# Performance work log

Measured on AMD Instinct MI355X. Metric: run time of the kernel, lower is better.

## Reference

```python
import jax, jax.numpy as jnp
import numpy as np


def setup_inputs() -> dict:
    key = jax.random.key(0)
    ks = jax.random.split(key, 7)
    B, S, IN, OUT = 4, 2048, 4096, 4096
    R_DEC, R_TR = 1024, 64
    return {
        "x": jax.random.normal(ks[0], (B, S, IN), dtype=jnp.float32),
        "siva_u_t": jax.random.normal(ks[1], (OUT, R_TR), dtype=jnp.float32) * 0.02,
        "siva_u_d": jax.random.normal(ks[2], (OUT, R_DEC - R_TR), dtype=jnp.float32) * 0.02,
        "siva_s": jax.random.uniform(ks[3], (R_DEC,), dtype=jnp.float32),
        "siva_v_t": jax.random.normal(ks[4], (R_TR, IN), dtype=jnp.float32) * 0.02,
        "siva_v_d": jax.random.normal(ks[5], (R_DEC - R_TR, IN), dtype=jnp.float32) * 0.02,
        "bias": jax.random.normal(ks[6], (OUT,), dtype=jnp.float32) * 0.02,
    }


def reference(x, siva_u_t, siva_u_d, siva_s, siva_v_t, siva_v_d, bias):
    # Faithful to torch: weight = (cat(U_t, U_d, dim=1) * S) @ cat(V_t, V_d, dim=0)
    siva_u = jnp.concatenate((siva_u_t, siva_u_d), axis=1)   # [out, r]
    siva_v = jnp.concatenate((siva_v_t, siva_v_d), axis=0)   # [r, in]
    weight = (siva_u * siva_s) @ siva_v                       # [out, in]
    # F.linear: x @ weight.T + bias
    return jnp.einsum("bsi,oi->bso", x, weight) + bias
```

## Files before the change

### kernel.cpp

```cpp
#include <hip/hip_runtime.h>
#include <cstdint>


#define BM 128
#define BN 128
#define BK 32

typedef __bf16 bf16x8 __attribute__((ext_vector_type(8)));
typedef float f32x4 __attribute__((ext_vector_type(4)));

__device__ __forceinline__ unsigned short f32_to_bf16(float f) {
    union { float f; uint32_t u; } v; v.f = f;
    uint32_t u = v.u;
    u += 0x7FFF + ((u >> 16) & 1);
    return (unsigned short)(u >> 16);
}

__global__ void cast_f32_bf16(const float* __restrict__ src,
                              unsigned short* __restrict__ dst, int n4) {
    int i = blockIdx.x * blockDim.x + threadIdx.x;
    if (i >= n4) return;
    float4 v = ((const float4*)src)[i];
    ushort4 o;
    o.x = f32_to_bf16(v.x); o.y = f32_to_bf16(v.y);
    o.z = f32_to_bf16(v.z); o.w = f32_to_bf16(v.w);
    ((ushort4*)dst)[i] = o;
}

__global__ void build_u(const float* __restrict__ u_t, const float* __restrict__ u_d,
                        const float* __restrict__ s, unsigned short* __restrict__ ub,
                        int n4) {
    int i = blockIdx.x * blockDim.x + threadIdx.x;
    if (i >= n4) return;
    int e = i * 4;
    int o = e >> 10;
    int r = e & 1023;
    float4 u;
    if (r < 64) u = *(const float4*)(u_t + (size_t)o * 64 + r);
    else        u = *(const float4*)(u_d + (size_t)o * 960 + (r - 64));
    float4 sv = *(const float4*)(s + r);
    ushort4 w;
    w.x = f32_to_bf16(u.x * sv.x);
    w.y = f32_to_bf16(u.y * sv.y);
    w.z = f32_to_bf16(u.z * sv.z);
    w.w = f32_to_bf16(u.w * sv.w);
    ((ushort4*)ub)[i] = w;
}

__device__ __forceinline__ void stage16(const unsigned short* g, unsigned short* l) {
    __builtin_amdgcn_global_load_lds(
        (const __attribute__((address_space(1))) uint32_t*)g,
        (__attribute__((address_space(3))) uint32_t*)l, 16, 0, 0);
}

__global__ __launch_bounds__(256, 4)
void gemm_a(const unsigned short* __restrict__ A, const unsigned short* __restrict__ B,
            float* __restrict__ Yp) {
    __shared__ unsigned short ldsA[BM * BK];
    __shared__ unsigned short ldsB[BN * BK];

    const int tid  = threadIdx.x;
    const int wave = tid >> 6, lane = tid & 63;
    const int wm = wave >> 1, wn = wave & 1;
    const int q = lane >> 4, l16 = lane & 15;

    const int b = blockIdx.x + (blockIdx.y << 3);
    const int c = b & 7;
    const int t = b >> 3;
    const int tx = t & 7;
    const int ty = ((t >> 3) << 3) + c;
    const int m0 = ty * BM, n0 = tx * BN;
    const int kbase = blockIdx.z * 2048;

    f32x4 acc[4][4] = {};

    const int rowc = tid >> 2;
    const int colc = (tid & 3) << 3;
    const unsigned short* pA0 = A + (size_t)(m0 + rowc) * 4096 + kbase + colc;
    const unsigned short* pA1 = pA0 + (size_t)64 * 4096;
    const unsigned short* pB0 = B + (size_t)(n0 + rowc) * 4096 + kbase + colc;
    const unsigned short* pB1 = pB0 + (size_t)64 * 4096;
    unsigned short* lA0 = ldsA + tid * 8;
    unsigned short* lA1 = ldsA + (tid + 256) * 8;
    unsigned short* lB0 = ldsB + tid * 8;
    unsigned short* lB1 = ldsB + (tid + 256) * 8;

    const int raBase = (wm * 64 + l16) * BK + q * 8;
    const int rbBase = (wn * 64 + l16) * BK + q * 8;

    for (int kt = 0; kt < 64; ++kt) {
        stage16(pA0, lA0);
        stage16(pA1, lA1);
        stage16(pB0, lB0);
        stage16(pB1, lB1);
        pA0 += BK; pA1 += BK; pB0 += BK; pB1 += BK;
        asm volatile("s_waitcnt vmcnt(0)" ::: "memory");
        __syncthreads();

        bf16x8 af[4], bfr[4];
#pragma unroll
        for (int i = 0; i < 4; ++i) {
            af[i]  = *(const bf16x8*)(ldsA + raBase + i * (16 * BK));
            bfr[i] = *(const bf16x8*)(ldsB + rbBase + i * (16 * BK));
        }
#pragma unroll
        for (int mt = 0; mt < 4; ++mt)
#pragma unroll
            for (int nt = 0; nt < 4; ++nt)
                acc[mt][nt] = __builtin_amdgcn_mfma_f32_16x16x32_bf16(
                    af[mt], bfr[nt], acc[mt][nt], 0, 0, 0);
        __syncthreads();
    }

    float* out = Yp + (size_t)blockIdx.z * 8192 * 1024;
#pragma unroll
    for (int mt = 0; mt < 4; ++mt)
#pragma unroll
        for (int nt = 0; nt < 4; ++nt) {
            const int col = n0 + wn * 64 + nt * 16 + l16;
            const int rbase = m0 + wm * 64 + mt * 16 + q * 4;
#pragma unroll
            for (int i = 0; i < 4; ++i)
                out[(size_t)(rbase + i) * 1024 + col] = acc[mt][nt][i];
        }
}

__global__ void reduce_y(const float* __restrict__ p0, const float* __restrict__ p1,
                         unsigned short* __restrict__ y, int n4) {
    int i = blockIdx.x * blockDim.x + threadIdx.x;
    if (i >= n4) return;
    float4 a = ((const float4*)p0)[i];
    float4 b = ((const float4*)p1)[i];
    ushort4 w;
    w.x = f32_to_bf16(a.x + b.x);
    w.y = f32_to_bf16(a.y + b.y);
    w.z = f32_to_bf16(a.z + b.z);
    w.w = f32_to_bf16(a.w + b.w);
    ((ushort4*)y)[i] = w;
}

__global__ __launch_bounds__(256, 4)
void gemm_b(const unsigned short* __restrict__ A, const unsigned short* __restrict__ B,
            float* __restrict__ C, const float* __restrict__ bias) {
    __shared__ unsigned short ldsA[BM * BK];
    __shared__ unsigned short ldsB[BN * BK];

    const int tid  = threadIdx.x;
    const int wave = tid >> 6, lane = tid & 63;
    const int wm = wave >> 1, wn = wave & 1;
    const int q = lane >> 4, l16 = lane & 15;

    const int b = blockIdx.x + (blockIdx.y << 5);
    const int c = b & 7;
    const int t = b >> 3;
    const int tx = t & 31;
    const int ty = ((t >> 5) << 3) + c;
    const int m0 = ty * BM, n0 = tx * BN;

    const int K = 1024, N = 4096;
    f32x4 acc[4][4] = {};

    const int rowc = tid >> 2;
    const int colc = (tid & 3) << 3;
    const unsigned short* pA0 = A + (size_t)(m0 + rowc) * K + colc;
    const unsigned short* pA1 = pA0 + (size_t)64 * K;
    const unsigned short* pB0 = B + (size_t)(n0 + rowc) * K + colc;
    const unsigned short* pB1 = pB0 + (size_t)64 * K;
    unsigned short* lA0 = ldsA + tid * 8;
    unsigned short* lA1 = ldsA + (tid + 256) * 8;
    unsigned short* lB0 = ldsB + tid * 8;
    unsigned short* lB1 = ldsB + (tid + 256) * 8;

    const int raBase = (wm * 64 + l16) * BK + q * 8;
    const int rbBase = (wn * 64 + l16) * BK + q * 8;

    for (int kt = 0; kt < K / BK; ++kt) {
        stage16(pA0, lA0);
        stage16(pA1, lA1);
        stage16(pB0, lB0);
        stage16(pB1, lB1);
        pA0 += BK; pA1 += BK; pB0 += BK; pB1 += BK;
        asm volatile("s_waitcnt vmcnt(0)" ::: "memory");
        __syncthreads();

        bf16x8 af[4], bfr[4];
#pragma unroll
        for (int i = 0; i < 4; ++i) {
            af[i]  = *(const bf16x8*)(ldsA + raBase + i * (16 * BK));
            bfr[i] = *(const bf16x8*)(ldsB + rbBase + i * (16 * BK));
        }
#pragma unroll
        for (int mt = 0; mt < 4; ++mt)
#pragma unroll
            for (int nt = 0; nt < 4; ++nt)
                acc[mt][nt] = __builtin_amdgcn_mfma_f32_16x16x32_bf16(
                    af[mt], bfr[nt], acc[mt][nt], 0, 0, 0);
        __syncthreads();
    }

#pragma unroll
    for (int mt = 0; mt < 4; ++mt)
#pragma unroll
        for (int nt = 0; nt < 4; ++nt) {
            const int col = n0 + wn * 64 + nt * 16 + l16;
            const int rbase = m0 + wm * 64 + mt * 16 + q * 4;
            const float bv = bias[col];
#pragma unroll
            for (int i = 0; i < 4; ++i)
                C[(size_t)(rbase + i) * N + col] = acc[mt][nt][i] + bv;
        }
}

extern "C" void kernel_launch(void* const* d_in, const int* in_sizes, int n_in,
                              void* d_out, int out_size, void* d_ws, size_t ws_size,
                              hipStream_t stream) {
    const float* x    = (const float*)d_in[0];
    const float* u_t  = (const float*)d_in[1];
    const float* u_d  = (const float*)d_in[2];
    const float* s    = (const float*)d_in[3];
    const float* v_t  = (const float*)d_in[4];
    const float* v_d  = (const float*)d_in[5];
    const float* bias = (const float*)d_in[6];
    float* out = (float*)d_out;

    const int M = 8192, IN = 4096, R = 1024, OUT = 4096;

    char* ws = (char*)d_ws;
    float*          Yp = (float*)ws;
    unsigned short* xb = (unsigned short*)(ws + (size_t)(64 << 20));
    unsigned short* Vb = (unsigned short*)(ws + (size_t)(128 << 20));
    unsigned short* Ub = (unsigned short*)(ws + (size_t)(136 << 20));
    unsigned short* Yb = (unsigned short*)(ws + (size_t)(144 << 20));

    {
        int n4 = M * IN / 4;
        cast_f32_bf16<<<(n4 + 255) / 256, 256, 0, stream>>>(x, xb, n4);
    }
    {
        int n4 = 64 * IN / 4;
        cast_f32_bf16<<<(n4 + 255) / 256, 256, 0, stream>>>(v_t, Vb, n4);
    }
    {
        int n4 = 960 * IN / 4;
        cast_f32_bf16<<<(n4 + 255) / 256, 256, 0, stream>>>(v_d, Vb + 64 * IN, n4);
    }
    {
        int n4 = OUT * R / 4;
        build_u<<<(n4 + 255) / 256, 256, 0, stream>>>(u_t, u_d, s, Ub, n4);
    }

    gemm_a<<<dim3(R / BN, M / BM, 2), 256, 0, stream>>>(xb, Vb, Yp);
    {
        int n4 = M * R / 4;
        reduce_y<<<(n4 + 255) / 256, 256, 0, stream>>>(Yp, Yp + (size_t)M * R, Yb, n4);
    }
    gemm_b<<<dim3(OUT / BN, M / BM), 256, 0, stream>>>(Yb, Ub, out, bias);
}
```

Measured before the change: 434.1 us.

## Replace both GEMMs with a double-buffered 256x256 tile kernel with swizzled LDS

Replaces the two 128x128 single-buffered GEMM kernels with one templated 256x256-tile, 512-thread kernel. It uses BK=64 split into two halves, double-buffered LDS with async global-to-LDS prefetch interleaved between MFMA phases, and XOR-swizzled LDS layout to avoid bank conflicts. It also adds s_setprio around MFMA bursts and a new block-index swizzle. This targets the load-wait-compute serialization and low arithmetic intensity of the old kernels, at the cost of higher register and LDS use and fewer resident blocks.

After: 413.9 us. -4.6%, faster.

```diff
diff --git a/kernel.cpp b/kernel.cpp
--- a/kernel.cpp
+++ b/kernel.cpp
@@ -1,10 +1,6 @@
 #include <hip/hip_runtime.h>
 #include <cstdint>
 
-
-#define BM 128
-#define BN 128
-#define BK 32
 
 typedef __bf16 bf16x8 __attribute__((ext_vector_type(8)));
 typedef float f32x4 __attribute__((ext_vector_type(4)));
@@ -47,84 +43,6 @@
     ((ushort4*)ub)[i] = w;
 }
 
-__device__ __forceinline__ void stage16(const unsigned short* g, unsigned short* l) {
-    __builtin_amdgcn_global_load_lds(
-        (const __attribute__((address_space(1))) uint32_t*)g,
-        (__attribute__((address_space(3))) uint32_t*)l, 16, 0, 0);
-}
-
-__global__ __launch_bounds__(256, 4)
-void gemm_a(const unsigned short* __restrict__ A, const unsigned short* __restrict__ B,
-            float* __restrict__ Yp) {
-    __shared__ unsigned short ldsA[BM * BK];
-    __shared__ unsigned short ldsB[BN * BK];
-
-    const int tid  = threadIdx.x;
-    const int wave = tid >> 6, lane = tid & 63;
-    const int wm = wave >> 1, wn = wave & 1;
-    const int q = lane >> 4, l16 = lane & 15;
-
-    const int b = blockIdx.x + (blockIdx.y << 3);
-    const int c = b & 7;
-    const int t = b >> 3;
-    const int tx = t & 7;
-    const int ty = ((t >> 3) << 3) + c;
-    const int m0 = ty * BM, n0 = tx * BN;
-    const int kbase = blockIdx.z * 2048;
-
-    f32x4 acc[4][4] = {};
-
-    const int rowc = tid >> 2;
-    const int colc = (tid & 3) << 3;
-    const unsigned short* pA0 = A + (size_t)(m0 + rowc) * 4096 + kbase + colc;
-    const unsigned short* pA1 = pA0 + (size_t)64 * 4096;
-    const unsigned short* pB0 = B + (size_t)(n0 + rowc) * 4096 + kbase + colc;
-    const unsigned short* pB1 = pB0 + (size_t)64 * 4096;
-    unsigned short* lA0 = ldsA + tid * 8;
-    unsigned short* lA1 = ldsA + (tid + 256) * 8;
-    unsigned short* lB0 = ldsB + tid * 8;
-    unsigned short* lB1 = ldsB + (tid + 256) * 8;
-
-    const int raBase = (wm * 64 + l16) * BK + q * 8;
-    const int rbBase = (wn * 64 + l16) * BK + q * 8;
-
-    for (int kt = 0; kt < 64; ++kt) {
-        stage16(pA0, lA0);
-        stage16(pA1, lA1);
-        stage16(pB0, lB0);
-        stage16(pB1, lB1);
-        pA0 += BK; pA1 += BK; pB0 += BK; pB1 += BK;
-        asm volatile("s_waitcnt vmcnt(0)" ::: "memory");
-        __syncthreads();
-
-        bf16x8 af[4], bfr[4];
-#pragma unroll
-        for (int i = 0; i < 4; ++i) {
-            af[i]  = *(const bf16x8*)(ldsA + raBase + i * (16 * BK));
-            bfr[i] = *(const bf16x8*)(ldsB + rbBase + i * (16 * BK));
-        }
-#pragma unroll
-        for (int mt = 0; mt < 4; ++mt)
-#pragma unroll
-            for (int nt = 0; nt < 4; ++nt)
-                acc[mt][nt] = __builtin_amdgcn_mfma_f32_16x16x32_bf16(
-                    af[mt], bfr[nt], acc[mt][nt], 0, 0, 0);
-        __syncthreads();
-    }
-
-    float* out = Yp + (size_t)blockIdx.z * 8192 * 1024;
-#pragma unroll
-    for (int mt = 0; mt < 4; ++mt)
-#pragma unroll
-        for (int nt = 0; nt < 4; ++nt) {
-            const int col = n0 + wn * 64 + nt * 16 + l16;
-            const int rbase = m0 + wm * 64 + mt * 16 + q * 4;
-#pragma unroll
-            for (int i = 0; i < 4; ++i)
-                out[(size_t)(rbase + i) * 1024 + col] = acc[mt][nt][i];
-        }
-}
-
 __global__ void reduce_y(const float* __restrict__ p0, const float* __restrict__ p1,
                          unsigned short* __restrict__ y, int n4) {
     int i = blockIdx.x * blockDim.x + threadIdx.x;
@@ -139,76 +57,154 @@
     ((ushort4*)y)[i] = w;
 }
 
-__global__ __launch_bounds__(256, 4)
-void gemm_b(const unsigned short* __restrict__ A, const unsigned short* __restrict__ B,
-            float* __restrict__ C, const float* __restrict__ bias) {
-    __shared__ unsigned short ldsA[BM * BK];
-    __shared__ unsigned short ldsB[BN * BK];
-
-    const int tid  = threadIdx.x;
-    const int wave = tid >> 6, lane = tid & 63;
-    const int wm = wave >> 1, wn = wave & 1;
+__device__ __forceinline__ void stage16(const unsigned short* g, unsigned short* l) {
+    __builtin_amdgcn_global_load_lds(
+        (const __attribute__((address_space(1))) uint32_t*)g,
+        (__attribute__((address_space(3))) uint32_t*)l, 16, 0, 0);
+}
+
+
+#define STAGE_A(bb, kh, t_) do {                                              \
+    const unsigned short* s_ = pAsrc + (t_) * 64 + (kh) * 32;                 \
+    unsigned short* d_ = ldsA_dst + (bb) * 32768 + (kh) * 8192;               \
+    stage16(s_, d_);                                                          \
+    stage16(s_ + (size_t)128 * LD, d_ + 4096);                                \
+} while (0)
+
+#define STAGE_B(bb, kh, t_) do {                                              \
+    const unsigned short* s_ = pBsrc + (t_) * 64 + (kh) * 32;                 \
+    unsigned short* d_ = ldsB_dst + (bb) * 32768 + (kh) * 8192;               \
+    stage16(s_, d_);                                                          \
+    stage16(s_ + (size_t)128 * LD, d_ + 4096);                                \
+} while (0)
+
+#define READ_AF(bb, ks, mh) do {                                              \
+    const unsigned short* p_ = lds + (bb) * 32768 + (ks) * 8192 + aoff + (mh) * 2048; \
+    af[0] = *(const bf16x8*)(p_);                                             \
+    af[1] = *(const bf16x8*)(p_ + 512);                                       \
+    af[2] = *(const bf16x8*)(p_ + 1024);                                      \
+    af[3] = *(const bf16x8*)(p_ + 1536);                                      \
+} while (0)
+
+#define READ_BF(bb, ks) do {                                                  \
+    const unsigned short* p_ = lds + (bb) * 32768 + 16384 + (ks) * 8192 + boff; \
+    bfr[0] = *(const bf16x8*)(p_);                                            \
+    bfr[1] = *(const bf16x8*)(p_ + 512);                                      \
+    bfr[2] = *(const bf16x8*)(p_ + 1024);                                     \
+    bfr[3] = *(const bf16x8*)(p_ + 1536);                                     \
+} while (0)
+
+#define MFMA16(mh) do {                                                       \
+    __builtin_amdgcn_s_barrier();                                             \
+    __builtin_amdgcn_sched_barrier(0);                                        \
+    __builtin_amdgcn_s_setprio(1);                                            \
+    _Pragma("unroll") for (int i_ = 0; i_ < 4; ++i_) {                        \
+        _Pragma("unroll") for (int n_ = 0; n_ < 4; ++n_) {                    \
+            acc[(mh) * 4 + i_][n_] = __builtin_amdgcn_mfma_f32_16x16x32_bf16( \
+                af[i_], bfr[n_], acc[(mh) * 4 + i_][n_], 0, 0, 0);            \
+        }                                                                     \
+    }                                                                         \
+    __builtin_amdgcn_s_setprio(0);                                            \
+    __builtin_amdgcn_sched_barrier(0);                                        \
+} while (0)
+
+#define PHASE_END do {                                                        \
+    __builtin_amdgcn_s_barrier();                                             \
+    __builtin_amdgcn_sched_barrier(0);                                        \
+} while (0)
+
+#define BODY(t_, bb) do {                                                     \
+    const int tp1 = (t_) + 1, tp2 = (t_) + 2;                                 \
+    bf16x8 af[4], bfr[4];                                                     \
+                                                          \
+    READ_AF(bb, 0, 0); READ_BF(bb, 0);                                        \
+    if (tp1 < KTILES) STAGE_A((bb) ^ 1, 1, tp1);                              \
+    MFMA16(0); PHASE_END;                                                     \
+                                                          \
+    READ_AF(bb, 0, 1);                                                        \
+    if (tp1 < KTILES) STAGE_B((bb) ^ 1, 1, tp1);                              \
+    MFMA16(1); PHASE_END;                                                     \
+                                                          \
+    READ_AF(bb, 1, 0); READ_BF(bb, 1);                                        \
+    if (tp2 < KTILES) STAGE_A((bb), 0, tp2);                                  \
+    MFMA16(0); PHASE_END;                                                     \
+                                                          \
+    READ_AF(bb, 1, 1);                                                        \
+    if (tp2 < KTILES) STAGE_B((bb), 0, tp2);                                  \
+    MFMA16(1);                                                                \
+    if (tp2 < KTILES)      asm volatile("s_waitcnt vmcnt(4)" ::: "memory");   \
+    else if (tp1 < KTILES) asm volatile("s_waitcnt vmcnt(0)" ::: "memory");   \
+    PHASE_END;                                                                \
+} while (0)
+
+template<int KTILES, int LD, int NTX, bool BIAS, int SPLITK>
+__global__ __launch_bounds__(512, 2)
+void gemm256(const unsigned short* __restrict__ A, const unsigned short* __restrict__ B,
+             float* __restrict__ C, const float* __restrict__ bias) {
+    static_assert((KTILES % 2) == 0 && KTILES >= 4, "KTILES even >= 4");
+    __shared__ unsigned short lds[65536];
+
+    const int tid = threadIdx.x;
+    const int wv = tid >> 6, lane = tid & 63;
+    const int wm = wv >> 2, wn = wv & 3;
     const int q = lane >> 4, l16 = lane & 15;
 
-    const int b = blockIdx.x + (blockIdx.y << 5);
-    const int c = b & 7;
-    const int t = b >> 3;
-    const int tx = t & 31;
-    const int ty = ((t >> 5) << 3) + c;
-    const int m0 = ty * BM, n0 = tx * BN;
-
-    const int K = 1024, N = 4096;
-    f32x4 acc[4][4] = {};
-
-    const int rowc = tid >> 2;
-    const int colc = (tid & 3) << 3;
-    const unsigned short* pA0 = A + (size_t)(m0 + rowc) * K + colc;
-    const unsigned short* pA1 = pA0 + (size_t)64 * K;
-    const unsigned short* pB0 = B + (size_t)(n0 + rowc) * K + colc;
-    const unsigned short* pB1 = pB0 + (size_t)64 * K;
-    unsigned short* lA0 = ldsA + tid * 8;
-    unsigned short* lA1 = ldsA + (tid + 256) * 8;
-    unsigned short* lB0 = ldsB + tid * 8;
-    unsigned short* lB1 = ldsB + (tid + 256) * 8;
-
-    const int raBase = (wm * 64 + l16) * BK + q * 8;
-    const int rbBase = (wn * 64 + l16) * BK + q * 8;
-
-    for (int kt = 0; kt < K / BK; ++kt) {
-        stage16(pA0, lA0);
-        stage16(pA1, lA1);
-        stage16(pB0, lB0);
-        stage16(pB1, lB1);
-        pA0 += BK; pA1 += BK; pB0 += BK; pB1 += BK;
-        asm volatile("s_waitcnt vmcnt(0)" ::: "memory");
-        __syncthreads();
-
-        bf16x8 af[4], bfr[4];
-#pragma unroll
-        for (int i = 0; i < 4; ++i) {
-            af[i]  = *(const bf16x8*)(ldsA + raBase + i * (16 * BK));
-            bfr[i] = *(const bf16x8*)(ldsB + rbBase + i * (16 * BK));
+    const int cpx = gridDim.x >> 3;
+    const int bswz = (blockIdx.x & 7) * cpx + (blockIdx.x >> 3);
+    const int tx = bswz % NTX, ty = bswz / NTX;
+    const int m0 = ty * 256, n0 = tx * 256;
+
+    const int z = blockIdx.z;
+    const unsigned short* Az = A + (size_t)z * SPLITK;
+    const unsigned short* Bz = B + (size_t)z * SPLITK;
+    float* Cz = C + (size_t)z * 8192 * (NTX * 256);
+
+    const int rowS = tid >> 2;
+    const int ccS  = (tid & 3) ^ ((tid >> 3) & 3);
+    const unsigned short* pAsrc = Az + (size_t)(m0 + rowS) * LD + ccS * 8;
+    const unsigned short* pBsrc = Bz + (size_t)(n0 + rowS) * LD + ccS * 8;
+    unsigned short* ldsA_dst = lds + tid * 8;
+    unsigned short* ldsB_dst = lds + 16384 + tid * 8;
+
+    const int xr = (l16 >> 1) & 3;
+    const int qx = (q ^ xr) * 8;
+    const int aoff = (wm * 128 + l16) * 32 + qx;
+    const int boff = (wn * 64 + l16) * 32 + qx;
+
+    f32x4 acc[8][4] = {};
+
+    STAGE_A(0, 0, 0); STAGE_B(0, 0, 0);
+    STAGE_A(0, 1, 0); STAGE_B(0, 1, 0);
+    STAGE_A(1, 0, 1); STAGE_B(1, 0, 1);
+    asm volatile("s_waitcnt vmcnt(4)" ::: "memory");
+    __builtin_amdgcn_s_barrier();
+    __builtin_amdgcn_sched_barrier(0);
+
+    for (int t = 0; t < KTILES; t += 2) {
+        BODY(t, 0);
+        BODY(t + 1, 1);
+    }
+
+    const int ldc = NTX * 256;
+    float bvv[4];
+    if (BIAS) {
+#pragma unroll
+        for (int nf = 0; nf < 4; ++nf) bvv[nf] = bias[n0 + wn * 64 + nf * 16 + l16];
+    }
+#pragma unroll
+    for (int mf = 0; mf < 8; ++mf) {
+#pragma unroll
+        for (int nf = 0; nf < 4; ++nf) {
+            const int col = n0 + wn * 64 + nf * 16 + l16;
+            const size_t rb = (size_t)(m0 + wm * 128 + mf * 16 + q * 4);
+#pragma unroll
+            for (int i = 0; i < 4; ++i) {
+                float v = acc[mf][nf][i];
+                if (BIAS) v += bvv[nf];
+                Cz[(rb + i) * ldc + col] = v;
+            }
         }
-#pragma unroll
-        for (int mt = 0; mt < 4; ++mt)
-#pragma unroll
-            for (int nt = 0; nt < 4; ++nt)
-                acc[mt][nt] = __builtin_amdgcn_mfma_f32_16x16x32_bf16(
-                    af[mt], bfr[nt], acc[mt][nt], 0, 0, 0);
-        __syncthreads();
-    }
-
-#pragma unroll
-    for (int mt = 0; mt < 4; ++mt)
-#pragma unroll
-        for (int nt = 0; nt < 4; ++nt) {
-            const int col = n0 + wn * 64 + nt * 16 + l16;
-            const int rbase = m0 + wm * 64 + mt * 16 + q * 4;
-            const float bv = bias[col];
-#pragma unroll
-            for (int i = 0; i < 4; ++i)
-                C[(size_t)(rbase + i) * N + col] = acc[mt][nt][i] + bv;
-        }
+    }
 }
 
 extern "C" void kernel_launch(void* const* d_in, const int* in_sizes, int n_in,
@@ -249,10 +245,10 @@
         build_u<<<(n4 + 255) / 256, 256, 0, stream>>>(u_t, u_d, s, Ub, n4);
     }
 
-    gemm_a<<<dim3(R / BN, M / BM, 2), 256, 0, stream>>>(xb, Vb, Yp);
+    gemm256<32, 4096, 4, false, 2048><<<dim3(128, 1, 2), 512, 0, stream>>>(xb, Vb, Yp, nullptr);
     {
         int n4 = M * R / 4;
         reduce_y<<<(n4 + 255) / 256, 256, 0, stream>>>(Yp, Yp + (size_t)M * R, Yb, n4);
     }
-    gemm_b<<<dim3(OUT / BN, M / BM), 256, 0, stream>>>(Yb, Ub, out, bias);
-}
+    gemm256<16, 1024, 16, true, 0><<<dim3(512, 1, 1), 512, 0, stream>>>(Yb, Ub, out, bias);
+}
```
